# Kernel optimization log

Hardware: AMD Instinct MI355X
Metric: run time of the kernel (lower is better)

The kernel has to match this reference:

```python
import jax, jax.numpy as jnp
import numpy as np

B, T, C = 4, 2048, 1024
H = 16
HD = C // H

def setup_inputs() -> dict:
    key = jax.random.key(0)
    k1, k2, k3 = jax.random.split(key, 3)
    x = jax.random.normal(k1, (B, T, C), dtype=jnp.float32)
    w_attn = jax.random.normal(k2, (C, 3 * C), dtype=jnp.float32) * 0.02
    b_attn = jnp.zeros((3 * C,), dtype=jnp.float32)
    w_proj = jax.random.normal(k3, (C, C), dtype=jnp.float32) * 0.02
    b_proj = jnp.zeros((C,), dtype=jnp.float32)
    return {"x": x, "w_attn": w_attn, "b_attn": b_attn, "w_proj": w_proj, "b_proj": b_proj}

def reference(x, w_attn, b_attn, w_proj, b_proj):
    Bx, Tx, Cx = x.shape
    qkv = x @ w_attn + b_attn                      # [B,T,3C]
    q, k, v = jnp.split(qkv, 3, axis=-1)
    # [B,T,C] -> [B,H,T,HD]
    q = q.reshape(Bx, Tx, H, HD).transpose(0, 2, 1, 3)
    k = k.reshape(Bx, Tx, H, HD).transpose(0, 2, 1, 3)
    v = v.reshape(Bx, Tx, H, HD).transpose(0, 2, 1, 3)
    scale = 1.0 / jnp.sqrt(jnp.asarray(HD, dtype=x.dtype))
    att = jnp.einsum('bhqd,bhkd->bhqk', q, k) * scale
    causal = jnp.tril(jnp.ones((Tx, Tx), dtype=bool))
    att = jnp.where(causal[None, None], att, jnp.finfo(att.dtype).min)
    att = jax.nn.softmax(att, axis=-1)
    y = jnp.einsum('bhqk,bhkd->bhqd', att, v)       # [B,H,T,HD]
    y = y.transpose(0, 2, 1, 3).reshape(Bx, Tx, Cx)
    return y @ w_proj + b_proj
```

## Files before the change

### kernel.cpp

```cpp
#include <hip/hip_runtime.h>
#include <hip/hip_bf16.h>

#define B_ 4
#define T_ 2048
#define C_ 1024
#define H_ 16
#define HD_ 64
#define BT_ (B_*T_)
#define C3_ (3*C_)
#define BHTD_ ((size_t)B_*H_*T_*HD_)

#define QSCALE 0.18033688011112042f

using u16 = unsigned short;
using u32 = unsigned int;
using bf16x8 = __attribute__((ext_vector_type(8))) short;
using f32x4  = __attribute__((ext_vector_type(4))) float;
using f32x16 = __attribute__((ext_vector_type(16))) float;
using u16x4  = __attribute__((ext_vector_type(4))) u16;
typedef int i32x2 __attribute__((ext_vector_type(2)));

#if __has_builtin(__builtin_amdgcn_exp2f)
#define EXP2(x) __builtin_amdgcn_exp2f(x)
#else
#define EXP2(x) exp2f(x)
#endif

__device__ __forceinline__ u16 f2bf(float f) {
  u32 u = __float_as_uint(f);
  u += 0x7fffu + ((u >> 16) & 1u);
  return (u16)(u >> 16);
}

__device__ __forceinline__ u32 cvtpk(float lo, float hi) {
  u32 r;
  asm("v_cvt_pk_bf16_f32 %0, %1, %2" : "=v"(r) : "v"(lo), "v"(hi));
  return r;
}

__device__ __forceinline__ void plswap(u32 &a, u32 &b) {
#if __has_builtin(__builtin_amdgcn_permlane32_swap)
  i32x2 r = __builtin_amdgcn_permlane32_swap((int)a, (int)b, false, false);
  a = (u32)r[0]; b = (u32)r[1];
#else
  asm volatile("v_permlane32_swap_b32 %0, %1" : "+v"(a), "+v"(b));
#endif
}

__device__ __forceinline__ float xmaxf(float x) {
  u32 a = __float_as_uint(x), b = a;
  plswap(a, b);
  return fmaxf(__uint_as_float(a), __uint_as_float(b));
}
__device__ __forceinline__ float xaddf(float x) {
  u32 a = __float_as_uint(x), b = a;
  plswap(a, b);
  return __uint_as_float(a) + __uint_as_float(b);
}

__device__ __forceinline__ void gload16(const void* g,
                                        __attribute__((address_space(3))) void* l) {
  __builtin_amdgcn_global_load_lds((const __attribute__((address_space(1))) void*)g,
                                   l, 16, 0, 0);
}

__global__ __launch_bounds__(256) void k_prep(const float* __restrict__ x,
                                              u16* __restrict__ xbf,
                                              const float* __restrict__ w_attn,
                                              u16* __restrict__ wat,
                                              const float* __restrict__ w_proj,
                                              u16* __restrict__ wpt) {
  __shared__ float t[32][33];
  int fb = blockIdx.x;
  if (fb < 8192) {
    size_t i = ((size_t)fb * 256 + threadIdx.x) * 4;
    f32x4 f = *(const f32x4*)(x + i);
    u16x4 o;
    o[0] = f2bf(f[0]); o[1] = f2bf(f[1]); o[2] = f2bf(f[2]); o[3] = f2bf(f[3]);
    *(u16x4*)(xbf + i) = o;
    return;
  }
  const float* w; u16* wt; int K, N, n0, k0;
  if (fb < 8192 + 3072) {
    int tb = fb - 8192;
    w = w_attn; wt = wat; K = C_; N = C3_;
    n0 = (tb % 96) * 32; k0 = (tb / 96) * 32;
  } else {
    int tb = fb - 8192 - 3072;
    w = w_proj; wt = wpt; K = C_; N = C_;
    n0 = (tb % 32) * 32; k0 = (tb / 32) * 32;
  }
  int tx = threadIdx.x & 31;
  int ty = threadIdx.x >> 5;
  #pragma unroll
  for (int r = 0; r < 4; ++r)
    t[ty + r*8][tx] = w[(size_t)(k0 + ty + r*8) * N + n0 + tx];
  __syncthreads();
  #pragma unroll
  for (int r = 0; r < 4; ++r)
    wt[(size_t)(n0 + ty + r*8) * K + k0 + tx] = f2bf(t[tx][ty + r*8]);
}

__global__ __launch_bounds__(256) void k_transpose_v(const u16* __restrict__ qkv3,
                                                     u16* __restrict__ dst) {
  __shared__ u16 t[64][72];
  int bh = blockIdx.y;
  int bb = bh >> 4, hh = bh & 15;
  int t0 = blockIdx.x * 64;
  const u16* s = qkv3 + (size_t)(bb*T_)*C3_ + 2*C_ + hh*64;
  u16* d = dst + (size_t)bh * HD_ * T_;
  int r = threadIdx.x >> 2, c0 = (threadIdx.x & 3) * 16;
  bf16x8 a0 = *(const bf16x8*)(s + (size_t)(t0 + r)*C3_ + c0);
  bf16x8 a1 = *(const bf16x8*)(s + (size_t)(t0 + r)*C3_ + c0 + 8);
  #pragma unroll
  for (int j = 0; j < 8; ++j) t[r][c0 + j] = (u16)a0[j];
  #pragma unroll
  for (int j = 0; j < 8; ++j) t[r][c0 + 8 + j] = (u16)a1[j];
  __syncthreads();
  bf16x8 b0, b1;
  #pragma unroll
  for (int j = 0; j < 8; ++j) b0[j] = (short)t[c0 + j][r];
  #pragma unroll
  for (int j = 0; j < 8; ++j) b1[j] = (short)t[c0 + 8 + j][r];
  *(bf16x8*)(d + (size_t)r*T_ + t0 + c0) = b0;
  *(bf16x8*)(d + (size_t)r*T_ + t0 + c0 + 8) = b1;
}

template<int EPI, int K>
__global__ __launch_bounds__(512) void k_gemm(const u16* __restrict__ A,
                                              const u16* __restrict__ Bt,
                                              const float* __restrict__ bias,
                                              void* __restrict__ outp) {
  __shared__ __align__(16) u16 lA[256*64];
  __shared__ __align__(16) u16 lB[128*64];
  int tid = threadIdx.x;
  int wave = tid >> 6, lane = tid & 63;
  int wr = wave >> 1, wc = wave & 1;
  int lrow = lane & 15, lgrp = lane >> 4;
  int bidf = blockIdx.y * gridDim.x + blockIdx.x;
  int xcd = bidf & 7, loc = bidf >> 3;
  int ypx = gridDim.y >> 3;
  int bx = loc / ypx;
  int by = xcd * ypx + (loc % ypx);
  int row0 = by * 256, col0 = bx * 128;

  f32x4 zero = {0.f, 0.f, 0.f, 0.f};
  f32x4 acc[4][4];
  #pragma unroll
  for (int m = 0; m < 4; ++m)
    #pragma unroll
    for (int n = 0; n < 4; ++n) acc[m][n] = zero;

  for (int kt = 0; kt < K; kt += 64) {
    #pragma unroll
    for (int it = 0; it < 4; ++it) {
      int c = tid + it*512;
      int r = c >> 3, sl = c & 7;
      int sk = sl ^ (r & 7);
      gload16(A + (size_t)(row0 + r)*K + kt + sk*8,
              (__attribute__((address_space(3))) char*)lA + it*8192 + wave*1024);
    }
    #pragma unroll
    for (int it = 0; it < 2; ++it) {
      int c = tid + it*512;
      int r = c >> 3, sl = c & 7;
      int sk = sl ^ (r & 7);
      gload16(Bt + (size_t)(col0 + r)*K + kt + sk*8,
              (__attribute__((address_space(3))) char*)lB + it*8192 + wave*1024);
    }
    __syncthreads();
    #pragma unroll
    for (int kk = 0; kk < 2; ++kk) {
      bf16x8 af[4], bfr[4];
      #pragma unroll
      for (int m = 0; m < 4; ++m) {
        int row = wr*64 + m*16 + lrow;
        af[m] = *(const bf16x8*)(lA + row*64 + (((kk*4 + lgrp) ^ (row & 7)))*8);
      }
      #pragma unroll
      for (int n = 0; n < 4; ++n) {
        int row = wc*64 + n*16 + lrow;
        bfr[n] = *(const bf16x8*)(lB + row*64 + (((kk*4 + lgrp) ^ (row & 7)))*8);
      }
      #pragma unroll
      for (int m = 0; m < 4; ++m)
        #pragma unroll
        for (int n = 0; n < 4; ++n)
          acc[m][n] = __builtin_amdgcn_mfma_f32_16x16x32_bf16(af[m], bfr[n], acc[m][n], 0, 0, 0);
    }
    __syncthreads();
  }

  #pragma unroll
  for (int m = 0; m < 4; ++m) {
    #pragma unroll
    for (int n = 0; n < 4; ++n) {
      int gcol = col0 + wc*64 + n*16 + lrow;
      float bv = bias[gcol];
      #pragma unroll
      for (int r = 0; r < 4; ++r) {
        int grow = row0 + wr*64 + m*16 + lgrp*4 + r;
        float val = acc[m][n][r] + bv;
        if (EPI == 0) {
          if (gcol < C_) val *= QSCALE;
          ((u16*)outp)[(size_t)grow*C3_ + gcol] = f2bf(val);
        } else {
          ((float*)outp)[(size_t)grow*C_ + gcol] = val;
        }
      }
    }
  }
}

__global__ __launch_bounds__(256, 2) void k_attn(const u16* __restrict__ qkv3,
                                                 const u16* __restrict__ vt,
                                                 u16* __restrict__ y) {
  __shared__ __align__(16) u16 Kl[2][64][72];
  __shared__ __align__(16) u16 Vl[2][64][72];
  int tid = threadIdx.x;
  int wave = tid >> 6, lane = tid & 63;
  int l31 = lane & 31, hi = lane >> 5;
  int bid = blockIdx.x;
  int head = bid & 63;
  int jA = bid >> 6;
  int jB = 15 - jA;
  int bidx = head >> 4, hh = head & 15;
  const u16* qb = qkv3 + (size_t)(bidx*T_)*C3_ + hh*64;
  const u16* kb = qkv3 + (size_t)(bidx*T_)*C3_ + C_ + hh*64;
  const u16* vb = vt + (size_t)head * HD_ * T_;

  int sr = tid >> 2;
  int sc = (tid & 3) * 16;

  f32x16 zero16 = {0.f,0.f,0.f,0.f,0.f,0.f,0.f,0.f,0.f,0.f,0.f,0.f,0.f,0.f,0.f,0.f};

  int qr0A = jA*128 + wave*32, qr0B = jB*128 + wave*32;
  bf16x8 qfA[4], qfB[4];
  {
    const u16* qrowA = qb + (size_t)(qr0A + l31)*C3_ + hi*8;
    const u16* qrowB = qb + (size_t)(qr0B + l31)*C3_ + hi*8;
    #pragma unroll
    for (int i = 0; i < 4; ++i) { qfA[i] = *(const bf16x8*)(qrowA + 16*i);
                                  qfB[i] = *(const bf16x8*)(qrowB + 16*i); }
  }
  f32x16 oA0 = zero16, oA1 = zero16, oB0 = zero16, oB1 = zero16;
  float mrunA = -1e30f, lrunA = 0.f, mrunB = -1e30f, lrunB = 0.f;
  int qgA = qr0A + l31, qgB = qr0B + l31;
  int ntA = 2*jA + 2, ntB = 2*jB + 2;

  auto step = [&](bf16x8 (&qf)[4], f32x16 &od0, f32x16 &od1,
                  float &mrun, float &lrun, int qg, int qr0, int kv0, int cb) {
    if (kv0 > qr0 + 31) return;
    bf16x8 kf[8], vf[8];
    #pragma unroll
    for (int i = 0; i < 4; ++i) {
      int cc = 16*i + 8*hi;
      kf[i]     = *(const bf16x8*)&Kl[cb][l31][cc];
      kf[4 + i] = *(const bf16x8*)&Kl[cb][l31 + 32][cc];
      vf[i]     = *(const bf16x8*)&Vl[cb][l31][cc];
      vf[4 + i] = *(const bf16x8*)&Vl[cb][l31 + 32][cc];
    }

    f32x16 s0 = zero16, s1 = zero16;
    __builtin_amdgcn_s_setprio(1);
    s0 = __builtin_amdgcn_mfma_f32_32x32x16_bf16(kf[0], qf[0], s0, 0, 0, 0);
    s1 = __builtin_amdgcn_mfma_f32_32x32x16_bf16(kf[4], qf[0], s1, 0, 0, 0);
    s0 = __builtin_amdgcn_mfma_f32_32x32x16_bf16(kf[1], qf[1], s0, 0, 0, 0);
    s1 = __builtin_amdgcn_mfma_f32_32x32x16_bf16(kf[5], qf[1], s1, 0, 0, 0);
    s0 = __builtin_amdgcn_mfma_f32_32x32x16_bf16(kf[2], qf[2], s0, 0, 0, 0);
    s1 = __builtin_amdgcn_mfma_f32_32x32x16_bf16(kf[6], qf[2], s1, 0, 0, 0);
    s0 = __builtin_amdgcn_mfma_f32_32x32x16_bf16(kf[3], qf[3], s0, 0, 0, 0);
    s1 = __builtin_amdgcn_mfma_f32_32x32x16_bf16(kf[7], qf[3], s1, 0, 0, 0);
    __builtin_amdgcn_s_setprio(0);

    if (kv0 + 63 > qr0) {
      #pragma unroll
      for (int r = 0; r < 16; ++r) {
        int kl2 = (r & 3) + 8*(r >> 2) + 4*hi;
        if (kv0 + kl2      > qg) s0[r] = -1e30f;
        if (kv0 + 32 + kl2 > qg) s1[r] = -1e30f;
      }
    }

    float tmx[16];
    #pragma unroll
    for (int i = 0; i < 16; ++i) tmx[i] = fmaxf(s0[i], s1[i]);
    #pragma unroll
    for (int off = 8; off > 0; off >>= 1)
      #pragma unroll
      for (int i = 0; i < 8; ++i)
        if (i < off) tmx[i] = fmaxf(tmx[i], tmx[i + off]);
    float pmax = xmaxf(tmx[0]);

    if (!__all(pmax <= mrun)) {
      float mnew = fmaxf(mrun, pmax);
      float ex = EXP2(mrun - mnew);
      mrun = mnew;
      lrun *= ex;
      #pragma unroll
      for (int i = 0; i < 16; ++i) { od0[i] *= ex; od1[i] *= ex; }
    }

    #pragma unroll
    for (int i = 0; i < 16; ++i) s0[i] = EXP2(s0[i] - mrun);
    #pragma unroll
    for (int i = 0; i < 16; ++i) s1[i] = EXP2(s1[i] - mrun);
    float u[16];
    #pragma unroll
    for (int i = 0; i < 16; ++i) u[i] = s0[i] + s1[i];
    #pragma unroll
    for (int off = 8; off > 0; off >>= 1)
      #pragma unroll
      for (int i = 0; i < 8; ++i)
        if (i < off) u[i] = u[i] + u[i + off];
    lrun += xaddf(u[0]);

    bf16x8 pf0, pf1, pf2, pf3;
    {
      u32 a0 = cvtpk(s0[0], s0[1]),   a1 = cvtpk(s0[2], s0[3]);
      u32 b0 = cvtpk(s0[4], s0[5]),   b1 = cvtpk(s0[6], s0[7]);
      plswap(a0, b0); plswap(a1, b1);
      u32 wa[4] = {a0, a1, b0, b1};
      __builtin_memcpy(&pf0, wa, 16);
    }
    {
      u32 a0 = cvtpk(s0[8], s0[9]),   a1 = cvtpk(s0[10], s0[11]);
      u32 b0 = cvtpk(s0[12], s0[13]), b1 = cvtpk(s0[14], s0[15]);
      plswap(a0, b0); plswap(a1, b1);
      u32 wa[4] = {a0, a1, b0, b1};
      __builtin_memcpy(&pf1, wa, 16);
    }
    {
      u32 a0 = cvtpk(s1[0], s1[1]),   a1 = cvtpk(s1[2], s1[3]);
      u32 b0 = cvtpk(s1[4], s1[5]),   b1 = cvtpk(s1[6], s1[7]);
      plswap(a0, b0); plswap(a1, b1);
      u32 wa[4] = {a0, a1, b0, b1};
      __builtin_memcpy(&pf2, wa, 16);
    }
    {
      u32 a0 = cvtpk(s1[8], s1[9]),   a1 = cvtpk(s1[10], s1[11]);
      u32 b0 = cvtpk(s1[12], s1[13]), b1 = cvtpk(s1[14], s1[15]);
      plswap(a0, b0); plswap(a1, b1);
      u32 wa[4] = {a0, a1, b0, b1};
      __builtin_memcpy(&pf3, wa, 16);
    }

    __builtin_amdgcn_s_setprio(1);
    od0 = __builtin_amdgcn_mfma_f32_32x32x16_bf16(vf[0], pf0, od0, 0, 0, 0);
    od0 = __builtin_amdgcn_mfma_f32_32x32x16_bf16(vf[1], pf1, od0, 0, 0, 0);
    od0 = __builtin_amdgcn_mfma_f32_32x32x16_bf16(vf[2], pf2, od0, 0, 0, 0);
    od0 = __builtin_amdgcn_mfma_f32_32x32x16_bf16(vf[3], pf3, od0, 0, 0, 0);
    od1 = __builtin_amdgcn_mfma_f32_32x32x16_bf16(vf[4], pf0, od1, 0, 0, 0);
    od1 = __builtin_amdgcn_mfma_f32_32x32x16_bf16(vf[5], pf1, od1, 0, 0, 0);
    od1 = __builtin_amdgcn_mfma_f32_32x32x16_bf16(vf[6], pf2, od1, 0, 0, 0);
    od1 = __builtin_amdgcn_mfma_f32_32x32x16_bf16(vf[7], pf3, od1, 0, 0, 0);
    __builtin_amdgcn_s_setprio(0);
  };

  {
    const u16* ks = kb + (size_t)sr*C3_ + sc;
    const u16* vs = vb + (size_t)sr*T_ + sc;
    bf16x8 k0 = *(const bf16x8*)ks, k1 = *(const bf16x8*)(ks + 8);
    bf16x8 v0 = *(const bf16x8*)vs, v1 = *(const bf16x8*)(vs + 8);
    *(bf16x8*)&Kl[0][sr][sc] = k0; *(bf16x8*)&Kl[0][sr][sc + 8] = k1;
    *(bf16x8*)&Vl[0][sr][sc] = v0; *(bf16x8*)&Vl[0][sr][sc + 8] = v1;
    __syncthreads();
  }

  for (int t = 0; t < ntB; ++t) {
    int kv0 = t*64;
    int cb = t & 1, nb = cb ^ 1;
    bool haveNext = (t + 1 < ntB);

    bf16x8 nk0, nk1, nv0, nv1;
    if (haveNext) {
      const u16* ks = kb + (size_t)(kv0 + 64 + sr)*C3_ + sc;
      const u16* vs = vb + (size_t)sr*T_ + (kv0 + 64) + sc;
      nk0 = *(const bf16x8*)ks; nk1 = *(const bf16x8*)(ks + 8);
      nv0 = *(const bf16x8*)vs; nv1 = *(const bf16x8*)(vs + 8);
    }

    if (t < ntA) step(qfA, oA0, oA1, mrunA, lrunA, qgA, qr0A, kv0, cb);
    step(qfB, oB0, oB1, mrunB, lrunB, qgB, qr0B, kv0, cb);

    if (haveNext) {
      *(bf16x8*)&Kl[nb][sr][sc] = nk0; *(bf16x8*)&Kl[nb][sr][sc + 8] = nk1;
      *(bf16x8*)&Vl[nb][sr][sc] = nv0; *(bf16x8*)&Vl[nb][sr][sc + 8] = nv1;
    }
    __syncthreads();
  }

  {
    float inv = 1.0f / lrunA;
    u16* yrow = y + ((size_t)(bidx*T_) + qr0A + l31)*C_ + hh*64;
    #pragma unroll
    for (int r = 0; r < 8; ++r) {
      int dp = ((2*r) & 3) + 8*(r >> 1) + 4*hi;
      *(u32*)(yrow + dp)      = cvtpk(oA0[2*r]*inv, oA0[2*r+1]*inv);
      *(u32*)(yrow + 32 + dp) = cvtpk(oA1[2*r]*inv, oA1[2*r+1]*inv);
    }
  }
  {
    float inv = 1.0f / lrunB;
    u16* yrow = y + ((size_t)(bidx*T_) + qr0B + l31)*C_ + hh*64;
    #pragma unroll
    for (int r = 0; r < 8; ++r) {
      int dp = ((2*r) & 3) + 8*(r >> 1) + 4*hi;
      *(u32*)(yrow + dp)      = cvtpk(oB0[2*r]*inv, oB0[2*r+1]*inv);
      *(u32*)(yrow + 32 + dp) = cvtpk(oB1[2*r]*inv, oB1[2*r+1]*inv);
    }
  }
}

extern "C" void kernel_launch(void* const* d_in, const int* in_sizes, int n_in,
                              void* d_out, int out_size, void* d_ws, size_t ws_size,
                              hipStream_t stream) {
  const float* x      = (const float*)d_in[0];
  const float* w_attn = (const float*)d_in[1];
  const float* b_attn = (const float*)d_in[2];
  const float* w_proj = (const float*)d_in[3];
  const float* b_proj = (const float*)d_in[4];

  char* ws = (char*)d_ws;
  size_t off = 0;
  auto walloc = [&](size_t bytes) -> void* {
    void* p = ws + off;
    off += (bytes + 255) & ~(size_t)255;
    return p;
  };
  u16* xbf  = (u16*)walloc((size_t)BT_ * C_ * 2);
  u16* wat  = (u16*)walloc((size_t)C3_ * C_ * 2);
  u16* wpt  = (u16*)walloc((size_t)C_ * C_ * 2);
  u16* qkv3 = (u16*)walloc((size_t)BT_ * C3_ * 2);
  u16* vT   = (u16*)walloc(BHTD_ * 2);
  u16* ybf = xbf;

  k_prep<<<dim3(12288), 256, 0, stream>>>(x, xbf, w_attn, wat, w_proj, wpt);
  k_gemm<0, C_><<<dim3(C3_/128, BT_/256), 512, 0, stream>>>(xbf, wat, b_attn, (void*)qkv3);
  k_transpose_v<<<dim3(T_/64, B_*H_), 256, 0, stream>>>(qkv3, vT);
  k_attn<<<dim3(512), 256, 0, stream>>>(qkv3, vT, ybf);
  k_gemm<1, C_><<<dim3(C_/128, BT_/256), 512, 0, stream>>>(ybf, wpt, b_proj, d_out);
}
```

Measured before the change: 165.8 us.

## Split attention KV range across two blocks and merge partial outputs

Doubles the attention grid so each query-tile pair is processed by two blocks, each covering half of the causal KV range. Each block writes an unnormalized bf16 partial output plus its running max and sum. A new merge kernel rescales and combines the two partials into the final attention output. This aims to raise parallelism and shorten each block's critical path, at the cost of extra global traffic, an extra launch, and bf16 rounding of the unnormalized partials.

```diff
diff --git a/kernel.cpp b/kernel.cpp
--- a/kernel.cpp
+++ b/kernel.cpp
@@ -30,6 +30,10 @@
   u32 u = __float_as_uint(f);
   u += 0x7fffu + ((u >> 16) & 1u);
   return (u16)(u >> 16);
+}
+
+__device__ __forceinline__ float bf2f(u16 v) {
+  return __uint_as_float(((u32)v) << 16);
 }
 
 __device__ __forceinline__ u32 cvtpk(float lo, float hi) {
@@ -214,7 +218,9 @@
 
 __global__ __launch_bounds__(256, 2) void k_attn(const u16* __restrict__ qkv3,
                                                  const u16* __restrict__ vt,
-                                                 u16* __restrict__ y) {
+                                                 u16* __restrict__ pO0,
+                                                 u16* __restrict__ pO1,
+                                                 float* __restrict__ pml) {
   __shared__ __align__(16) u16 Kl[2][64][72];
   __shared__ __align__(16) u16 Vl[2][64][72];
   int tid = threadIdx.x;
@@ -222,12 +228,14 @@
   int l31 = lane & 31, hi = lane >> 5;
   int bid = blockIdx.x;
   int head = bid & 63;
-  int jA = bid >> 6;
+  int jA = (bid >> 6) & 7;
+  int half = bid >> 9;
   int jB = 15 - jA;
   int bidx = head >> 4, hh = head & 15;
   const u16* qb = qkv3 + (size_t)(bidx*T_)*C3_ + hh*64;
   const u16* kb = qkv3 + (size_t)(bidx*T_)*C3_ + C_ + hh*64;
   const u16* vb = vt + (size_t)head * HD_ * T_;
+  u16* pO = half ? pO1 : pO0;
 
   int sr = tid >> 2;
   int sc = (tid & 3) * 16;
@@ -246,7 +254,10 @@
   f32x16 oA0 = zero16, oA1 = zero16, oB0 = zero16, oB1 = zero16;
   float mrunA = -1e30f, lrunA = 0.f, mrunB = -1e30f, lrunB = 0.f;
   int qgA = qr0A + l31, qgB = qr0B + l31;
-  int ntA = 2*jA + 2, ntB = 2*jB + 2;
+  int ntA = 2*jA + 2, ntB = 32 - 2*jA;
+  int sp = (jA <= 3) ? (15 - 2*jA) : 8;
+  int tbeg = half ? sp : 0;
+  int tend = half ? ntB : sp;
 
   auto step = [&](bf16x8 (&qf)[4], f32x16 &od0, f32x16 &od1,
                   float &mrun, float &lrun, int qg, int qr0, int kv0, int cb) {
@@ -358,19 +369,20 @@
   };
 
   {
-    const u16* ks = kb + (size_t)sr*C3_ + sc;
-    const u16* vs = vb + (size_t)sr*T_ + sc;
+    const u16* ks = kb + (size_t)(tbeg*64 + sr)*C3_ + sc;
+    const u16* vs = vb + (size_t)sr*T_ + tbeg*64 + sc;
     bf16x8 k0 = *(const bf16x8*)ks, k1 = *(const bf16x8*)(ks + 8);
     bf16x8 v0 = *(const bf16x8*)vs, v1 = *(const bf16x8*)(vs + 8);
-    *(bf16x8*)&Kl[0][sr][sc] = k0; *(bf16x8*)&Kl[0][sr][sc + 8] = k1;
-    *(bf16x8*)&Vl[0][sr][sc] = v0; *(bf16x8*)&Vl[0][sr][sc + 8] = v1;
+    int b0i = tbeg & 1;
+    *(bf16x8*)&Kl[b0i][sr][sc] = k0; *(bf16x8*)&Kl[b0i][sr][sc + 8] = k1;
+    *(bf16x8*)&Vl[b0i][sr][sc] = v0; *(bf16x8*)&Vl[b0i][sr][sc + 8] = v1;
     __syncthreads();
   }
 
-  for (int t = 0; t < ntB; ++t) {
+  for (int t = tbeg; t < tend; ++t) {
     int kv0 = t*64;
     int cb = t & 1, nb = cb ^ 1;
-    bool haveNext = (t + 1 < ntB);
+    bool haveNext = (t + 1 < tend);
 
     bf16x8 nk0, nk1, nv0, nv1;
     if (haveNext) {
@@ -391,25 +403,60 @@
   }
 
   {
-    float inv = 1.0f / lrunA;
-    u16* yrow = y + ((size_t)(bidx*T_) + qr0A + l31)*C_ + hh*64;
+    u16* prow = pO + ((size_t)(bidx*T_) + qr0A + l31)*C_ + hh*64;
     #pragma unroll
     for (int r = 0; r < 8; ++r) {
       int dp = ((2*r) & 3) + 8*(r >> 1) + 4*hi;
-      *(u32*)(yrow + dp)      = cvtpk(oA0[2*r]*inv, oA0[2*r+1]*inv);
-      *(u32*)(yrow + 32 + dp) = cvtpk(oA1[2*r]*inv, oA1[2*r+1]*inv);
+      *(u32*)(prow + dp)      = cvtpk(oA0[2*r], oA0[2*r+1]);
+      *(u32*)(prow + 32 + dp) = cvtpk(oA1[2*r], oA1[2*r+1]);
+    }
+    if (hi == 0) {
+      float* q = pml + (((size_t)(bidx*T_) + qr0A + l31)*H_ + hh)*4 + half*2;
+      q[0] = mrunA; q[1] = lrunA;
     }
   }
   {
-    float inv = 1.0f / lrunB;
-    u16* yrow = y + ((size_t)(bidx*T_) + qr0B + l31)*C_ + hh*64;
+    u16* prow = pO + ((size_t)(bidx*T_) + qr0B + l31)*C_ + hh*64;
     #pragma unroll
     for (int r = 0; r < 8; ++r) {
       int dp = ((2*r) & 3) + 8*(r >> 1) + 4*hi;
-      *(u32*)(yrow + dp)      = cvtpk(oB0[2*r]*inv, oB0[2*r+1]*inv);
-      *(u32*)(yrow + 32 + dp) = cvtpk(oB1[2*r]*inv, oB1[2*r+1]*inv);
-    }
-  }
+      *(u32*)(prow + dp)      = cvtpk(oB0[2*r], oB0[2*r+1]);
+      *(u32*)(prow + 32 + dp) = cvtpk(oB1[2*r], oB1[2*r+1]);
+    }
+    if (hi == 0) {
+      float* q = pml + (((size_t)(bidx*T_) + qr0B + l31)*H_ + hh)*4 + half*2;
+      q[0] = mrunB; q[1] = lrunB;
+    }
+  }
+}
+
+__global__ __launch_bounds__(256) void k_merge(const u16* __restrict__ pO0,
+                                               const u16* __restrict__ pO1,
+                                               const float* __restrict__ pml,
+                                               u16* __restrict__ y) {
+  int idx = blockIdx.x * 256 + threadIdx.x;
+  int row = idx >> 7;
+  int c8 = idx & 127;
+  int head = c8 >> 3;
+  const float* q = pml + ((size_t)row*H_ + head)*4;
+  float m0 = q[0], l0 = q[1], m1 = q[2], l1 = q[3];
+  float M = fmaxf(m0, m1);
+  float e0 = EXP2(m0 - M), e1 = EXP2(m1 - M);
+  float inv = 1.0f / (l0*e0 + l1*e1);
+  e0 *= inv; e1 *= inv;
+  size_t off = (size_t)idx * 8;
+  bf16x8 a = *(const bf16x8*)(pO0 + off);
+  bf16x8 b = *(const bf16x8*)(pO1 + off);
+  u32 w[4];
+  #pragma unroll
+  for (int p = 0; p < 4; ++p) {
+    float lo = bf2f((u16)a[2*p])     * e0 + bf2f((u16)b[2*p])     * e1;
+    float hi = bf2f((u16)a[2*p + 1]) * e0 + bf2f((u16)b[2*p + 1]) * e1;
+    w[p] = cvtpk(lo, hi);
+  }
+  bf16x8 out;
+  __builtin_memcpy(&out, w, 16);
+  *(bf16x8*)(y + off) = out;
 }
 
 extern "C" void kernel_launch(void* const* d_in, const int* in_sizes, int n_in,
@@ -428,16 +475,20 @@
     off += (bytes + 255) & ~(size_t)255;
     return p;
   };
-  u16* xbf  = (u16*)walloc((size_t)BT_ * C_ * 2);
-  u16* wat  = (u16*)walloc((size_t)C3_ * C_ * 2);
-  u16* wpt  = (u16*)walloc((size_t)C_ * C_ * 2);
-  u16* qkv3 = (u16*)walloc((size_t)BT_ * C3_ * 2);
-  u16* vT   = (u16*)walloc(BHTD_ * 2);
-  u16* ybf = xbf;
+  u16*   xbf  = (u16*)walloc((size_t)BT_ * C_ * 2);
+  u16*   wat  = (u16*)walloc((size_t)C3_ * C_ * 2);
+  u16*   wpt  = (u16*)walloc((size_t)C_ * C_ * 2);
+  u16*   qkv3 = (u16*)walloc((size_t)BT_ * C3_ * 2);
+  u16*   vT   = (u16*)walloc(BHTD_ * 2);
+  u16*   pO1  = (u16*)walloc((size_t)BT_ * C_ * 2);
+  float* pml  = (float*)walloc((size_t)BT_ * H_ * 4 * 4);
+  u16*   ybf  = (u16*)walloc((size_t)BT_ * C_ * 2);
+  u16*   pO0  = xbf;
 
   k_prep<<<dim3(12288), 256, 0, stream>>>(x, xbf, w_attn, wat, w_proj, wpt);
   k_gemm<0, C_><<<dim3(C3_/128, BT_/256), 512, 0, stream>>>(xbf, wat, b_attn, (void*)qkv3);
   k_transpose_v<<<dim3(T_/64, B_*H_), 256, 0, stream>>>(qkv3, vT);
-  k_attn<<<dim3(512), 256, 0, stream>>>(qkv3, vT, ybf);
+  k_attn<<<dim3(1024), 256, 0, stream>>>(qkv3, vT, pO0, pO1, pml);
+  k_merge<<<dim3((BT_*C_/8)/256), 256, 0, stream>>>(pO0, pO1, pml, ybf);
   k_gemm<1, C_><<<dim3(C_/128, BT_/256), 512, 0, stream>>>(ybf, wpt, b_proj, d_out);
 }
```

After: 187.7 us. 1.13x slower.
